# Kernel optimization log

Hardware: AMD Instinct MI355X
Metric: run time of the kernel (lower is better)

The kernel has to match this reference:

```python
import jax, jax.numpy as jnp
import numpy as np


def setup_inputs() -> dict:
    key = jax.random.key(0)
    k1, k2 = jax.random.split(key)
    B, S, H = 8, 4096, 1024
    sequence_output = jax.random.normal(k1, (B, S, H), dtype=jnp.float32)
    # labels in {0,1}: no -100 padding so the mask-compaction has a static shape
    sent_token_mask = jax.random.randint(k2, (B, S), 0, 2, dtype=jnp.int64)
    return {"sequence_output": sequence_output, "sent_token_mask": sent_token_mask}


def reference(sequence_output, sent_token_mask):
    B, S, H = sequence_output.shape
    # mask compaction: all positions valid (labels in {0,1}), so it's a reshape
    sent_features = sequence_output.reshape(B * S, H)  # [B*S, H]

    labels = sent_token_mask  # [B, S]
    # seg_id assigned BEFORE processing each label; increments AFTER label==0
    inc = (labels == 0).astype(jnp.int32).reshape(B * S)
    within = jnp.cumsum(inc) - inc  # exclusive prefix sum of increments
    # extra increment at end of each example whose last label == 1
    extra = (labels[:, -1] == 1).astype(jnp.int32)  # [B]
    extra_off = jnp.cumsum(extra) - extra           # exclusive over examples
    topic_segment_ids = within.reshape(B, S) + extra_off[:, None]
    return sent_features, topic_segment_ids.reshape(B * S)
```

## Files before the change

kernel.cpp:

```cpp
#include <hip/hip_runtime.h>

constexpr int Bn  = 8;
constexpr int Sn  = 4096;
constexpr int Nn  = Bn * Sn;
constexpr int Hn  = 1024;

constexpr int TPB = 256;
constexpr int NW  = TPB / 64;
constexpr int PER = Nn / TPB;

constexpr size_t FEAT_ELEMS = (size_t)Nn * Hn;
constexpr size_t FEAT_VEC4  = FEAT_ELEMS / 4;
constexpr int    VEC_PER_T  = 8;
constexpr int    COPY_BLOCKS = (int)(FEAT_VEC4 / ((size_t)TPB * VEC_PER_T));

typedef float v4f __attribute__((ext_vector_type(4)));

__global__ __launch_bounds__(TPB) void fused_kernel(const float* __restrict__ seq,
                                                    const int* __restrict__ labels,
                                                    float* __restrict__ out) {
    if (blockIdx.x > 0) {
        const v4f* __restrict__ src = reinterpret_cast<const v4f*>(seq);
        v4f* __restrict__ dst       = reinterpret_cast<v4f*>(out);
        const size_t base = (size_t)(blockIdx.x - 1) * (TPB * VEC_PER_T) + threadIdx.x;
        v4f r[VEC_PER_T];
#pragma unroll
        for (int i = 0; i < VEC_PER_T; ++i)
            r[i] = __builtin_nontemporal_load(&src[base + (size_t)i * TPB]);
#pragma unroll
        for (int i = 0; i < VEC_PER_T; ++i)
            __builtin_nontemporal_store(r[i], &dst[base + (size_t)i * TPB]);
        return;
    }

    __shared__ int wave_sums[NW];
    __shared__ int extra_off_sh[Bn];

    float* __restrict__ seg_out = out + FEAT_ELEMS;

    const int tid  = threadIdx.x;
    const int lane = tid & 63;
    const int wave = tid >> 6;
    const int base = tid * PER;

    const int4* l4 = reinterpret_cast<const int4*>(labels + base);
    int sum = 0;
#pragma unroll
    for (int i = 0; i < PER / 4; ++i) {
        int4 v = l4[i];
        sum += (v.x == 0) + (v.y == 0) + (v.z == 0) + (v.w == 0);
    }

    int incl = sum;
#pragma unroll
    for (int off = 1; off < 64; off <<= 1) {
        int u = __shfl_up(incl, off, 64);
        if (lane >= off) incl += u;
    }
    if (lane == 63) wave_sums[wave] = incl;

    if (tid == 0) {
        int acc = 0;
#pragma unroll
        for (int b = 0; b < Bn; ++b) {
            extra_off_sh[b] = acc;
            acc += (labels[b * Sn + Sn - 1] == 1);
        }
    }
    __syncthreads();

    if (wave == 0) {
        int v = (lane < NW) ? wave_sums[lane] : 0;
#pragma unroll
        for (int off = 1; off < NW; off <<= 1) {
            int u = __shfl_up(v, off, 64);
            if (lane >= off) v += u;
        }
        if (lane < NW) wave_sums[lane] = v;
    }
    __syncthreads();

    int excl = (wave ? wave_sums[wave - 1] : 0) + (incl - sum);
#pragma unroll
    for (int i = 0; i < PER / 4; ++i) {
        int4 v = l4[i];
        int idx = base + 4 * i;
        int eo  = extra_off_sh[idx >> 12];
        seg_out[idx + 0] = (float)(excl + eo); excl += (v.x == 0);
        eo = extra_off_sh[(idx + 1) >> 12];
        seg_out[idx + 1] = (float)(excl + eo); excl += (v.y == 0);
        eo = extra_off_sh[(idx + 2) >> 12];
        seg_out[idx + 2] = (float)(excl + eo); excl += (v.z == 0);
        eo = extra_off_sh[(idx + 3) >> 12];
        seg_out[idx + 3] = (float)(excl + eo); excl += (v.w == 0);
    }
}

extern "C" void kernel_launch(void* const* d_in, const int* in_sizes, int n_in,
                              void* d_out, int out_size, void* d_ws, size_t ws_size,
                              hipStream_t stream) {
    const float* seq    = (const float*)d_in[0];
    const int*   labels = (const int*)d_in[1];
    float*       out    = (float*)d_out;

    fused_kernel<<<COPY_BLOCKS + 1, TPB, 0, stream>>>(seq, labels, out);
}
```

Measured before the change: 219.4 us.

## Restructure segment-id scan for coalesced label loads and vectorized stores

The single scan block now reads labels in a strided, coalesced int4 pattern instead of giving each thread one contiguous 128-element range. It computes per-32-lane group counts, scans them in shared memory, then does a half-wave shuffle scan per iteration and writes float4 results with nontemporal stores. The aim is to shorten the serial tail of block 0, which previously issued uncoalesced scalar stores and strided loads. It adds extra shuffle work and shared-memory syncs.

```diff
diff --git a/kernel.cpp b/kernel.cpp
--- a/kernel.cpp
+++ b/kernel.cpp
@@ -7,7 +7,8 @@
 
 constexpr int TPB = 256;
 constexpr int NW  = TPB / 64;
-constexpr int PER = Nn / TPB;
+constexpr int G4    = Nn / 4;
+constexpr int ITERS = G4 / TPB;
 
 constexpr size_t FEAT_ELEMS = (size_t)Nn * Hn;
 constexpr size_t FEAT_VEC4  = FEAT_ELEMS / 4;
@@ -33,31 +34,27 @@
         return;
     }
 
+    __shared__ int range_pre[TPB];
     __shared__ int wave_sums[NW];
     __shared__ int extra_off_sh[Bn];
 
-    float* __restrict__ seg_out = out + FEAT_ELEMS;
-
     const int tid  = threadIdx.x;
     const int lane = tid & 63;
+    const int hl   = lane & 31;
     const int wave = tid >> 6;
-    const int base = tid * PER;
 
-    const int4* l4 = reinterpret_cast<const int4*>(labels + base);
-    int sum = 0;
+    const int4* __restrict__ lab4 = reinterpret_cast<const int4*>(labels);
+    v4f* __restrict__ seg4 = reinterpret_cast<v4f*>(out + FEAT_ELEMS);
+
+#pragma unroll 4
+    for (int i = 0; i < ITERS; ++i) {
+        const int g = i * TPB + tid;
+        int4 v = lab4[g];
+        int c = (v.x == 0) + (v.y == 0) + (v.z == 0) + (v.w == 0);
 #pragma unroll
-    for (int i = 0; i < PER / 4; ++i) {
-        int4 v = l4[i];
-        sum += (v.x == 0) + (v.y == 0) + (v.z == 0) + (v.w == 0);
+        for (int k = 1; k < 32; k <<= 1) c += __shfl_xor(c, k, 32);
+        if (hl == 0) range_pre[g >> 5] = c;
     }
-
-    int incl = sum;
-#pragma unroll
-    for (int off = 1; off < 64; off <<= 1) {
-        int u = __shfl_up(incl, off, 64);
-        if (lane >= off) incl += u;
-    }
-    if (lane == 63) wave_sums[wave] = incl;
 
     if (tid == 0) {
         int acc = 0;
@@ -67,6 +64,16 @@
             acc += (labels[b * Sn + Sn - 1] == 1);
         }
     }
+    __syncthreads();
+
+    const int s = range_pre[tid];
+    int incl = s;
+#pragma unroll
+    for (int off = 1; off < 64; off <<= 1) {
+        int u = __shfl_up(incl, off, 64);
+        if (lane >= off) incl += u;
+    }
+    if (lane == 63) wave_sums[wave] = incl;
     __syncthreads();
 
     if (wave == 0) {
@@ -80,19 +87,28 @@
     }
     __syncthreads();
 
-    int excl = (wave ? wave_sums[wave - 1] : 0) + (incl - sum);
+    range_pre[tid] = (wave ? wave_sums[wave - 1] : 0) + (incl - s);
+    __syncthreads();
+
+#pragma unroll 4
+    for (int i = 0; i < ITERS; ++i) {
+        const int g = i * TPB + tid;
+        int4 v = lab4[g];
+        const int f0 = (v.x == 0), f1 = (v.y == 0), f2 = (v.z == 0), f3 = (v.w == 0);
+        const int c = f0 + f1 + f2 + f3;
+        int pc = c;
 #pragma unroll
-    for (int i = 0; i < PER / 4; ++i) {
-        int4 v = l4[i];
-        int idx = base + 4 * i;
-        int eo  = extra_off_sh[idx >> 12];
-        seg_out[idx + 0] = (float)(excl + eo); excl += (v.x == 0);
-        eo = extra_off_sh[(idx + 1) >> 12];
-        seg_out[idx + 1] = (float)(excl + eo); excl += (v.y == 0);
-        eo = extra_off_sh[(idx + 2) >> 12];
-        seg_out[idx + 2] = (float)(excl + eo); excl += (v.z == 0);
-        eo = extra_off_sh[(idx + 3) >> 12];
-        seg_out[idx + 3] = (float)(excl + eo); excl += (v.w == 0);
+        for (int off = 1; off < 32; off <<= 1) {
+            int u = __shfl_up(pc, off, 32);
+            if (hl >= off) pc += u;
+        }
+        const int base = range_pre[g >> 5] + extra_off_sh[g >> 10] + (pc - c);
+        v4f r;
+        r.x = (float)base;
+        r.y = (float)(base + f0);
+        r.z = (float)(base + f0 + f1);
+        r.w = (float)(base + f0 + f1 + f2);
+        __builtin_nontemporal_store(r, &seg4[g]);
     }
 }
 
```

Result: slower. 233.4 us (+6.4%).
